# Optimization experiments

Hardware: AMD Instinct MI355X
Metric: run time of the kernel (lower is better)

Reference implementation:

```python
import jax, jax.numpy as jnp
import numpy as np
import math

GROUPS = 32  # min(256 // 4, 32)
EPS = 1e-5

def group_norm(x, w, b):
    B, C, H, W = x.shape
    xg = x.reshape(B, GROUPS, C // GROUPS, H, W)
    mean = jnp.mean(xg, axis=(2, 3, 4), keepdims=True)
    var = jnp.var(xg, axis=(2, 3, 4), keepdims=True)
    xn = ((xg - mean) * jax.lax.rsqrt(var + EPS)).reshape(B, C, H, W)
    return xn * w[None, :, None, None] + b[None, :, None, None]

def nin(x, W, b):
    # 1x1 projection: [B,C,H,W] x [C,D] -> [B,D,H,W]
    return jnp.einsum('bchw,cd->bdhw', x, W) + b[None, :, None, None]

def setup_inputs() -> dict:
    key = jax.random.key(0)
    ks = jax.random.split(key, 5)
    C = 256
    scale = 1.0 / math.sqrt(C)
    return {
        'x': jax.random.normal(ks[0], (4, C, 64, 64), dtype=jnp.float32),
        'gn_w': jnp.ones((C,), jnp.float32),
        'gn_b': jnp.zeros((C,), jnp.float32),
        'Wq': jax.random.normal(ks[1], (C, C), jnp.float32) * scale,
        'bq': jnp.zeros((C,), jnp.float32),
        'Wk': jax.random.normal(ks[2], (C, C), jnp.float32) * scale,
        'bk': jnp.zeros((C,), jnp.float32),
        'Wv': jax.random.normal(ks[3], (C, C), jnp.float32) * scale,
        'bv': jnp.zeros((C,), jnp.float32),
        'Wp': jax.random.normal(ks[4], (C, C), jnp.float32) * scale,
        'bp': jnp.zeros((C,), jnp.float32),
    }

def reference(x, gn_w, gn_b, Wq, bq, Wk, bk, Wv, bv, Wp, bp):
    B, C, H, W = x.shape
    h = group_norm(x, gn_w, gn_b)
    q = nin(h, Wq, bq).reshape(B, C, H * W)
    k = nin(h, Wk, bk).reshape(B, C, H * W)
    v = nin(h, Wv, bv).reshape(B, C, H * W)
    # attention logits: [B, HW, HW]
    w = jnp.einsum('bcn,bcm->bnm', q, k) * (C ** -0.5)
    w = jax.nn.softmax(w, axis=-1)
    h_out = jnp.einsum('bnm,bcm->bcn', w, v).reshape(B, C, H, W)
    h_out = nin(h_out, Wp, bp)
    out = x + h_out
    return out / math.sqrt(2.0)  # skip_rescale=True
```

## Files before the change

### kernel.cpp

```cpp
#include <hip/hip_runtime.h>
#include <math.h>


#define BB 4
#define CCH 256
#define NSP 4096
#define EPSV 1e-5f
#define ATTN_SCALE 0.0625f
#define RSQRT2 0.70710678118654752440f
#define KSPLIT 2
#define TILES_PER_PART 32

typedef __attribute__((ext_vector_type(8))) short bf16x8;
typedef __attribute__((ext_vector_type(4))) float f32x4;

typedef __attribute__((address_space(1))) void gvoid;
typedef __attribute__((address_space(3))) void lvoid;
__device__ __forceinline__ void dma16(const void* g, void* l) {
  __builtin_amdgcn_global_load_lds((gvoid*)g, (lvoid*)l, 16, 0, 0);
}

__device__ __forceinline__ short f2bf(float f) {
  union { float f; unsigned u; } a; a.f = f;
  unsigned r = a.u + 0x7fffu + ((a.u >> 16) & 1u);
  return (short)(r >> 16);
}
__device__ __forceinline__ float bf2f(short s) {
  union { unsigned u; float f; } a;
  a.u = ((unsigned)(unsigned short)s) << 16;
  return a.f;
}
__device__ __forceinline__ unsigned cvt_pk_bf16(float lo, float hi) {
  unsigned r;
  asm("v_cvt_pk_bf16_f32 %0, %1, %2" : "=v"(r) : "v"(lo), "v"(hi));
  return r;
}

__global__ __launch_bounds__(256) void gn_stats(
    const float* __restrict__ x, float* __restrict__ stats) {
  int b = blockIdx.x >> 5;
  int g = blockIdx.x & 31;
  size_t base = ((size_t)b * CCH + (size_t)g * 8) * NSP;
  const float4* xv = (const float4*)(x + base);
  int tid = threadIdx.x;
  float s = 0.f, ss = 0.f;
  for (int i = tid; i < 8192; i += 256) {
    float4 v = xv[i];
    s += (v.x + v.y) + (v.z + v.w);
    ss += (v.x * v.x + v.y * v.y) + (v.z * v.z + v.w * v.w);
  }
#pragma unroll
  for (int off = 32; off > 0; off >>= 1) {
    s += __shfl_down(s, off, 64);
    ss += __shfl_down(ss, off, 64);
  }
  __shared__ float rs[4], rss[4];
  int wv = tid >> 6;
  if ((tid & 63) == 0) { rs[wv] = s; rss[wv] = ss; }
  __syncthreads();
  if (tid == 0) {
    float S = rs[0] + rs[1] + rs[2] + rs[3];
    float SS = rss[0] + rss[1] + rss[2] + rss[3];
    float mean = S * (1.f / 32768.f);
    float var = SS * (1.f / 32768.f) - mean * mean;
    stats[(b * 32 + g) * 2 + 0] = mean;
    stats[(b * 32 + g) * 2 + 1] = rsqrtf(var + EPSV);
  }
}

__global__ __launch_bounds__(256) void prep_w(
    const float* __restrict__ Wq, const float* __restrict__ Wk,
    const float* __restrict__ Wv, const float* __restrict__ Wp,
    short* __restrict__ wts) {
  __shared__ float T[64][65];
  int c0 = blockIdx.x * 64, d0 = blockIdx.y * 64;
  int wz = blockIdx.z;
  const float* W = (wz == 0) ? Wq : (wz == 1) ? Wk : (wz == 2) ? Wv : Wp;
  short* wt = wts + (size_t)wz * CCH * CCH;
  int tid = threadIdx.x;
#pragma unroll
  for (int i = 0; i < 16; ++i) {
    int idx = tid + 256 * i;
    int row = idx >> 6, col = idx & 63;
    T[row][col] = W[(size_t)(c0 + row) * CCH + d0 + col];
  }
  __syncthreads();
#pragma unroll
  for (int i = 0; i < 16; ++i) {
    int idx = tid + 256 * i;
    int dr = idx >> 6, cc = idx & 63;
    wt[(size_t)(d0 + dr) * CCH + c0 + cc] = f2bf(T[cc][dr]);
  }
}

__global__ __launch_bounds__(256) void qkvg_kernel(
    const float* __restrict__ x, const float* __restrict__ stats,
    const float* __restrict__ gw, const float* __restrict__ gb,
    const short* __restrict__ wqt, const short* __restrict__ wkt,
    const short* __restrict__ wvt,
    const float* __restrict__ bq, const float* __restrict__ bk,
    const float* __restrict__ bv,
    short* __restrict__ qo, short* __restrict__ ko, short* __restrict__ vo) {
  __shared__ __align__(16) unsigned char smem[52224];
  float (*Ts)[68] = (float(*)[68])smem;
  float* aco = (float*)(smem + 17408);
  float* bco = aco + 256;
  short* Hs = (short*)(smem + 19456);
  short* Fo = (short*)smem;

  int bx = blockIdx.x;
  int b = bx & 3, n0 = (bx >> 2) * 64;
  int tid = threadIdx.x;
  {
    int g = tid >> 3;
    float mean = stats[(b * 32 + g) * 2 + 0];
    float rstd = stats[(b * 32 + g) * 2 + 1];
    float a = gw[tid] * rstd;
    aco[tid] = a;
    bco[tid] = gb[tid] - mean * a;
  }
  __syncthreads();
  const float* xb = x + (size_t)b * CCH * NSP;
  for (int p = 0; p < 4; ++p) {
    int c0 = p * 64;
#pragma unroll
    for (int i = 0; i < 4; ++i) {
      int crow = (tid >> 4) + i * 16;
      int c = c0 + crow;
      float4 v = *(const float4*)&xb[(size_t)c * NSP + n0 + (tid & 15) * 4];
      float a = aco[c], bb = bco[c];
      v.x = v.x * a + bb; v.y = v.y * a + bb;
      v.z = v.z * a + bb; v.w = v.w * a + bb;
      *(float4*)&Ts[crow][(tid & 15) * 4] = v;
    }
    __syncthreads();
    {
      int n = tid >> 2, seg = tid & 3;
#pragma unroll
      for (int u = 0; u < 2; ++u) {
        int cb = seg * 16 + u * 8;
        bf16x8 r;
#pragma unroll
        for (int j = 0; j < 8; ++j) r[j] = f2bf(Ts[cb + j][n]);
        int chunk = (c0 + cb) >> 3;
        *(bf16x8*)(Hs + n * 256 + ((chunk ^ (n & 7)) * 8)) = r;
      }
    }
    __syncthreads();
  }
  int w = tid >> 6, lane = tid & 63, quad = lane >> 4, l16 = lane & 15;
  bf16x8 a_h[8];
  {
    int row = w * 16 + l16;
#pragma unroll
    for (int kc = 0; kc < 8; ++kc)
      a_h[kc] = *(bf16x8*)(Hs + row * 256 + (((kc * 4 + quad) ^ (row & 7)) * 8));
  }
  __syncthreads();
  for (int op = 0; op < 3; ++op) {
    const short* wt = (op == 0) ? wqt : (op == 1) ? wkt : wvt;
    const float* bias = (op == 0) ? bq : (op == 1) ? bk : bv;
    f32x4 acc[16];
#pragma unroll
    for (int mb = 0; mb < 16; ++mb) acc[mb] = (f32x4){0.f, 0.f, 0.f, 0.f};
#pragma unroll 4
    for (int mb = 0; mb < 16; ++mb) {
      const short* wp = wt + (size_t)(mb * 16 + l16) * CCH + quad * 8;
#pragma unroll
      for (int kc = 0; kc < 8; ++kc) {
        bf16x8 af = *(const bf16x8*)(wp + kc * 32);
        acc[mb] = __builtin_amdgcn_mfma_f32_16x16x32_bf16(af, a_h[kc], acc[mb], 0, 0, 0);
      }
    }
    int n = n0 + w * 16 + l16;
    if (op == 2) {
      short* ob = vo + (size_t)b * CCH * NSP;
      int mm = n & 63, m0_ = n & ~63;
      int mb_ = mm >> 4, qq = (mm >> 2) & 3, rr2 = mm & 3;
      int lc = (mb_ & 1) * 4 + qq;
      int jj = (mb_ >> 1) * 4 + rr2;
      int basen = m0_ + jj;
#pragma unroll
      for (int mb = 0; mb < 16; ++mb)
#pragma unroll
        for (int r = 0; r < 4; ++r) {
          int d = mb * 16 + quad * 4 + r;
          ob[(size_t)d * NSP + basen + ((lc ^ (d & 7)) << 3)] =
              f2bf(acc[mb][r] + bias[d]);
        }
    } else {
      float sc = (op == 0) ? ATTN_SCALE : 1.f;
      int nl = w * 16 + l16;
#pragma unroll
      for (int mb = 0; mb < 16; ++mb)
#pragma unroll
        for (int r = 0; r < 4; ++r) {
          int d = mb * 16 + quad * 4 + r;
          Fo[nl * 264 + d] = f2bf((acc[mb][r] + bias[d]) * sc);
        }
      __syncthreads();
      short* ob = ((op == 0) ? qo : ko) + (size_t)b * NSP * CCH;
#pragma unroll
      for (int it = 0; it < 2; ++it) {
        int idx = tid + 256 * it;
        int row = idx >> 3, seg = idx & 7, r7 = row & 7;
        short* dst = ob + (size_t)(n0 + row) * CCH + seg * 32;
#pragma unroll
        for (int i = 0; i < 4; ++i) {
          int xch = seg * 4 + i;
          int cs = (xch & 24) | ((xch & 7) ^ r7);
          *(bf16x8*)(dst + i * 8) = *(bf16x8*)(Fo + row * 264 + cs * 8);
        }
      }
      __syncthreads();
    }
  }
}

__global__ __launch_bounds__(512, 1) void attn_kernel(
    const short* __restrict__ q, const short* __restrict__ k,
    const short* __restrict__ v, short* __restrict__ po,
    float* __restrict__ pm, float* __restrict__ pl) {
  __shared__ __align__(16) unsigned char smem[65536];
  short* Ks = (short*)smem;
  short* Vs = (short*)(smem + 32768);
  short* Fo = (short*)smem;

  int bx = blockIdx.x;
  int b = bx & 3;
  int n0 = ((bx >> 2) & 31) << 7;
  int kh = bx >> 7;
  const short* qb = q + (size_t)b * NSP * CCH;
  const short* kb = k + (size_t)b * NSP * CCH;
  const char*  vbB = (const char*)(v + (size_t)b * CCH * NSP);
  int tid = threadIdx.x;
  int w = tid >> 6, lane = tid & 63, quad = lane >> 4, l16 = lane & 15;
  int mbase = kh * TILES_PER_PART * 64;

#pragma unroll
  for (int i = 0; i < 4; ++i) {
    int off = tid * 16 + i * 8192;
    int c = off >> 7, inrow = off & 127;
    dma16(vbB + (size_t)c * (NSP * 2) + (size_t)mbase * 2 + inrow,
          (char*)Vs + off);
  }
#pragma unroll
  for (int i = 0; i < 4; ++i) {
    int off = tid * 16 + i * 8192;
    dma16((const char*)(qb + (size_t)n0 * CCH) + off, (char*)Ks + off);
  }
  __syncthreads();
  bf16x8 a_q[8];
  if ((w >> 2) == 0) {
    int row = (w & 3) * 16 + l16;
#pragma unroll
    for (int kc = 0; kc < 8; ++kc)
      a_q[kc] = *(bf16x8*)(Ks + row * 256 + (((kc * 4 + quad) ^ (row & 7)) * 8));
  }
  __syncthreads();
#pragma unroll
  for (int i = 0; i < 4; ++i) {
    int off = tid * 16 + i * 8192;
    dma16((const char*)(qb + (size_t)(n0 + 64) * CCH) + off, (char*)Ks + off);
  }
  __syncthreads();
  if ((w >> 2) == 1) {
    int row = (w & 3) * 16 + l16;
#pragma unroll
    for (int kc = 0; kc < 8; ++kc)
      a_q[kc] = *(bf16x8*)(Ks + row * 256 + (((kc * 4 + quad) ^ (row & 7)) * 8));
  }
  __syncthreads();
#pragma unroll
  for (int i = 0; i < 4; ++i) {
    int off = tid * 16 + i * 8192;
    dma16((const char*)(kb + (size_t)mbase * CCH) + off, (char*)Ks + off);
  }
  __syncthreads();

  f32x4 accO[16];
#pragma unroll
  for (int cb = 0; cb < 16; ++cb) accO[cb] = (f32x4){0.f, 0.f, 0.f, 0.f};
  float m_run = -1e30f, l_run = 0.f;
  int pc0 = quad ^ (l16 & 7);
  int pc1 = (4 + quad) ^ (l16 & 7);

#pragma unroll 1
  for (int t = 0; t < TILES_PER_PART; ++t) {
    f32x4 s[4];
#pragma unroll
    for (int mb = 0; mb < 4; ++mb) s[mb] = (f32x4){0.f, 0.f, 0.f, 0.f};
    __builtin_amdgcn_s_setprio(1);
#pragma unroll
    for (int kc = 0; kc < 8; ++kc) {
#pragma unroll
      for (int mb = 0; mb < 4; ++mb) {
        int row = mb * 16 + l16;
        bf16x8 kf = *(bf16x8*)(Ks + row * 256 + (((kc * 4 + quad) ^ (row & 7)) * 8));
        s[mb] = __builtin_amdgcn_mfma_f32_16x16x32_bf16(kf, a_q[kc], s[mb], 0, 0, 0);
      }
    }
    __builtin_amdgcn_s_setprio(0);
    __syncthreads();
    if (t < TILES_PER_PART - 1) {
      const char* kp = (const char*)(kb + (size_t)(mbase + (t + 1) * 64) * CCH);
#pragma unroll
      for (int i = 0; i < 4; ++i) {
        int off = tid * 16 + i * 8192;
        dma16(kp + off, (char*)Ks + off);
      }
    }
    float mx = -1e30f;
#pragma unroll
    for (int mb = 0; mb < 4; ++mb)
#pragma unroll
      for (int r = 0; r < 4; ++r) mx = fmaxf(mx, s[mb][r]);
    mx = fmaxf(mx, __shfl_xor(mx, 16));
    mx = fmaxf(mx, __shfl_xor(mx, 32));
    if (!__all(mx - m_run <= 8.f)) {
      float mnew = fmaxf(m_run, mx);
      float alpha = __expf(m_run - mnew);
#pragma unroll
      for (int cb = 0; cb < 16; ++cb) accO[cb] *= alpha;
      l_run *= alpha;
      m_run = mnew;
    }
    float ls = 0.f;
#pragma unroll
    for (int mb = 0; mb < 4; ++mb)
#pragma unroll
      for (int r = 0; r < 4; ++r) {
        float p = __expf(s[mb][r] - m_run);
        ls += p;
        s[mb][r] = p;
      }
    ls += __shfl_xor(ls, 16);
    ls += __shfl_xor(ls, 32);
    l_run += ls;
    union { unsigned u[4]; bf16x8 v; } pw0, pw1;
    pw0.u[0] = cvt_pk_bf16(s[0][0], s[0][1]);
    pw0.u[1] = cvt_pk_bf16(s[0][2], s[0][3]);
    pw0.u[2] = cvt_pk_bf16(s[2][0], s[2][1]);
    pw0.u[3] = cvt_pk_bf16(s[2][2], s[2][3]);
    pw1.u[0] = cvt_pk_bf16(s[1][0], s[1][1]);
    pw1.u[1] = cvt_pk_bf16(s[1][2], s[1][3]);
    pw1.u[2] = cvt_pk_bf16(s[3][0], s[3][1]);
    pw1.u[3] = cvt_pk_bf16(s[3][2], s[3][3]);
    __builtin_amdgcn_s_setprio(1);
#pragma unroll
    for (int cb = 0; cb < 16; ++cb) {
      bf16x8 vf = *(bf16x8*)(Vs + (cb * 16 + l16) * 64 + pc0 * 8);
      accO[cb] = __builtin_amdgcn_mfma_f32_16x16x32_bf16(vf, pw0.v, accO[cb], 0, 0, 0);
    }
#pragma unroll
    for (int cb = 0; cb < 16; ++cb) {
      bf16x8 vf = *(bf16x8*)(Vs + (cb * 16 + l16) * 64 + pc1 * 8);
      accO[cb] = __builtin_amdgcn_mfma_f32_16x16x32_bf16(vf, pw1.v, accO[cb], 0, 0, 0);
    }
    __builtin_amdgcn_s_setprio(0);
    __syncthreads();
    if (t < TILES_PER_PART - 1) {
      int m0 = mbase + (t + 1) * 64;
#pragma unroll
      for (int i = 0; i < 4; ++i) {
        int off = tid * 16 + i * 8192;
        int c = off >> 7, inrow = off & 127;
        dma16(vbB + (size_t)c * (NSP * 2) + (size_t)m0 * 2 + inrow,
              (char*)Vs + off);
      }
    }
  }
  size_t sbase = ((size_t)kh * BB + b) * NSP + n0;
  if (quad == 0) {
    pm[sbase + w * 16 + l16] = m_run;
    pl[sbase + w * 16 + l16] = l_run;
  }
  float linv = 1.f / l_run;
  short* ob = po + ((size_t)kh * BB + b) * NSP * CCH;
#pragma unroll
  for (int p = 0; p < 2; ++p) {
    __syncthreads();
    if ((w >> 2) == p) {
      int nloc = (w & 3) * 16 + l16;
#pragma unroll
      for (int cb = 0; cb < 16; ++cb)
#pragma unroll
        for (int r = 0; r < 4; ++r)
          Fo[nloc * 264 + cb * 16 + quad * 4 + r] = f2bf(accO[cb][r] * linv);
    }
    __syncthreads();
    int row = tid >> 3, seg = tid & 7;
    short* dst = ob + (size_t)(n0 + p * 64 + row) * CCH + seg * 32;
#pragma unroll
    for (int i = 0; i < 4; ++i)
      *(bf16x8*)(dst + i * 8) = *(bf16x8*)(Fo + row * 264 + seg * 32 + i * 8);
  }
}

__global__ __launch_bounds__(256) void proj_kernel(
    const short* __restrict__ po, const float* __restrict__ pm,
    const float* __restrict__ pl, const short* __restrict__ wpt,
    const float* __restrict__ bp, const float* __restrict__ x,
    float* __restrict__ out) {
  int n0 = blockIdx.x * 64;
  int dh = blockIdx.y * 128;
  int b = blockIdx.z;
  int tid = threadIdx.x;
  int w = tid >> 6, lane = tid & 63, quad = lane >> 4, l16 = lane & 15;
  int n = n0 + w * 16 + l16;

  float wgt[KSPLIT];
  {
    float m[KSPLIT];
    float M = -1e30f;
#pragma unroll
    for (int s = 0; s < KSPLIT; ++s) {
      m[s] = pm[((size_t)s * BB + b) * NSP + n];
      M = fmaxf(M, m[s]);
    }
    float wsum = 0.f;
#pragma unroll
    for (int s = 0; s < KSPLIT; ++s) {
      wgt[s] = __expf(m[s] - M) * pl[((size_t)s * BB + b) * NSP + n];
      wsum += wgt[s];
    }
    float linv = 1.f / wsum;
#pragma unroll
    for (int s = 0; s < KSPLIT; ++s) wgt[s] *= linv;
  }

  f32x4 acc[8];
#pragma unroll
  for (int mb = 0; mb < 8; ++mb) acc[mb] = (f32x4){0.f, 0.f, 0.f, 0.f};

  const short* pob = po + ((size_t)b * NSP + n) * CCH;
#pragma unroll 2
  for (int kc = 0; kc < 8; ++kc) {
    int coff = kc * 32 + quad * 8;
    float e[8];
#pragma unroll
    for (int i = 0; i < 8; ++i) e[i] = 0.f;
#pragma unroll
    for (int s = 0; s < KSPLIT; ++s) {
      bf16x8 f = *(const bf16x8*)(pob + (size_t)s * BB * NSP * CCH + coff);
#pragma unroll
      for (int i = 0; i < 8; ++i) e[i] += wgt[s] * bf2f(f[i]);
    }
    bf16x8 bm;
#pragma unroll
    for (int i = 0; i < 8; ++i) bm[i] = f2bf(e[i]);
#pragma unroll
    for (int mb = 0; mb < 8; ++mb) {
      bf16x8 af = *(const bf16x8*)(wpt + (size_t)(dh + mb * 16 + l16) * CCH + coff);
      acc[mb] = __builtin_amdgcn_mfma_f32_16x16x32_bf16(af, bm, acc[mb], 0, 0, 0);
    }
  }
#pragma unroll
  for (int mb = 0; mb < 8; ++mb) {
#pragma unroll
    for (int r = 0; r < 4; ++r) {
      int d = dh + mb * 16 + quad * 4 + r;
      size_t off = ((size_t)b * CCH + d) * NSP + n;
      out[off] = (acc[mb][r] + bp[d] + x[off]) * RSQRT2;
    }
  }
}

extern "C" void kernel_launch(void* const* d_in, const int* in_sizes, int n_in,
                              void* d_out, int out_size, void* d_ws, size_t ws_size,
                              hipStream_t stream) {
  const float* x  = (const float*)d_in[0];
  const float* gw = (const float*)d_in[1];
  const float* gb = (const float*)d_in[2];
  const float* Wq = (const float*)d_in[3];
  const float* bq = (const float*)d_in[4];
  const float* Wk = (const float*)d_in[5];
  const float* bk = (const float*)d_in[6];
  const float* Wv = (const float*)d_in[7];
  const float* bv = (const float*)d_in[8];
  const float* Wp = (const float*)d_in[9];
  const float* bp = (const float*)d_in[10];
  float* out = (float*)d_out;

  const size_t SZ = (size_t)BB * CCH * NSP;
  short* qb  = (short*)d_ws;
  short* kb  = qb + SZ;
  short* vb  = kb + SZ;
  short* poT = vb + SZ;
  float* pm  = (float*)(poT + (size_t)KSPLIT * SZ);
  float* pl  = pm + (size_t)KSPLIT * BB * NSP;
  float* stats = pl + (size_t)KSPLIT * BB * NSP;
  short* wts = (short*)(stats + BB * 64);
  short* wqt = wts;
  short* wkt = wts + (size_t)CCH * CCH;
  short* wvt = wts + (size_t)2 * CCH * CCH;
  short* wpt = wts + (size_t)3 * CCH * CCH;

  gn_stats<<<dim3(BB * 32), dim3(256), 0, stream>>>(x, stats);
  prep_w<<<dim3(4, 4, 4), dim3(256), 0, stream>>>(Wq, Wk, Wv, Wp, wts);
  qkvg_kernel<<<dim3(256), dim3(256), 0, stream>>>(
      x, stats, gw, gb, wqt, wkt, wvt, bq, bk, bv, qb, kb, vb);
  attn_kernel<<<dim3(BB * 32 * KSPLIT), dim3(512), 0, stream>>>(
      qb, kb, vb, poT, pm, pl);
  proj_kernel<<<dim3(64, 2, BB), dim3(256), 0, stream>>>(
      poT, pm, pl, wpt, bp, x, out);
}
```

Baseline: 289.0 us.

## Double-buffer K/V in LDS and software-pipeline QK^T one tile ahead

The attention kernel doubles its LDS to hold two K and two V tiles. It computes the QK^T scores for the next tile while the softmax and PV MFMAs for the current tile run, and prefetches K two tiles ahead and V one tile ahead. This cuts the loop to one barrier per iteration and is meant to hide global-load latency and let matrix work overlap the softmax math. In exchange it uses 128KB of LDS and extra registers for the held score tile.

```diff
diff --git a/kernel.cpp b/kernel.cpp
--- a/kernel.cpp
+++ b/kernel.cpp
@@ -221,10 +221,12 @@
     const short* __restrict__ q, const short* __restrict__ k,
     const short* __restrict__ v, short* __restrict__ po,
     float* __restrict__ pm, float* __restrict__ pl) {
-  __shared__ __align__(16) unsigned char smem[65536];
-  short* Ks = (short*)smem;
-  short* Vs = (short*)(smem + 32768);
-  short* Fo = (short*)smem;
+  __shared__ __align__(16) unsigned char smem[131072];
+  short* Ks0 = (short*)smem;
+  short* Ks1 = (short*)(smem + 32768);
+  short* Vs0 = (short*)(smem + 65536);
+  short* Vs1 = (short*)(smem + 98304);
+  short* Fo  = (short*)smem;
 
   int bx = blockIdx.x;
   int b = bx & 3;
@@ -237,46 +239,54 @@
   int w = tid >> 6, lane = tid & 63, quad = lane >> 4, l16 = lane & 15;
   int mbase = kh * TILES_PER_PART * 64;
 
+  bf16x8 a_q[8];
+#pragma unroll
+  for (int p = 0; p < 2; ++p) {
+#pragma unroll
+    for (int i = 0; i < 4; ++i) {
+      int off = tid * 16 + i * 8192;
+      dma16((const char*)(qb + (size_t)(n0 + p * 64) * CCH) + off,
+            (char*)Ks0 + off);
+    }
+    __syncthreads();
+    if ((w >> 2) == p) {
+      int row = (w & 3) * 16 + l16;
+#pragma unroll
+      for (int kc = 0; kc < 8; ++kc)
+        a_q[kc] = *(bf16x8*)(Ks0 + row * 256 + (((kc * 4 + quad) ^ (row & 7)) * 8));
+    }
+    __syncthreads();
+  }
+
 #pragma unroll
   for (int i = 0; i < 4; ++i) {
     int off = tid * 16 + i * 8192;
+    dma16((const char*)(kb + (size_t)mbase * CCH) + off, (char*)Ks0 + off);
     int c = off >> 7, inrow = off & 127;
     dma16(vbB + (size_t)c * (NSP * 2) + (size_t)mbase * 2 + inrow,
-          (char*)Vs + off);
-  }
+          (char*)Vs0 + off);
+  }
+  __syncthreads();
 #pragma unroll
   for (int i = 0; i < 4; ++i) {
     int off = tid * 16 + i * 8192;
-    dma16((const char*)(qb + (size_t)n0 * CCH) + off, (char*)Ks + off);
-  }
-  __syncthreads();
-  bf16x8 a_q[8];
-  if ((w >> 2) == 0) {
-    int row = (w & 3) * 16 + l16;
-#pragma unroll
-    for (int kc = 0; kc < 8; ++kc)
-      a_q[kc] = *(bf16x8*)(Ks + row * 256 + (((kc * 4 + quad) ^ (row & 7)) * 8));
-  }
-  __syncthreads();
-#pragma unroll
-  for (int i = 0; i < 4; ++i) {
-    int off = tid * 16 + i * 8192;
-    dma16((const char*)(qb + (size_t)(n0 + 64) * CCH) + off, (char*)Ks + off);
-  }
-  __syncthreads();
-  if ((w >> 2) == 1) {
-    int row = (w & 3) * 16 + l16;
-#pragma unroll
-    for (int kc = 0; kc < 8; ++kc)
-      a_q[kc] = *(bf16x8*)(Ks + row * 256 + (((kc * 4 + quad) ^ (row & 7)) * 8));
-  }
-  __syncthreads();
-#pragma unroll
-  for (int i = 0; i < 4; ++i) {
-    int off = tid * 16 + i * 8192;
-    dma16((const char*)(kb + (size_t)mbase * CCH) + off, (char*)Ks + off);
-  }
-  __syncthreads();
+    dma16((const char*)(kb + (size_t)(mbase + 64) * CCH) + off,
+          (char*)Ks1 + off);
+  }
+  f32x4 s_prev[4];
+#pragma unroll
+  for (int mb = 0; mb < 4; ++mb) s_prev[mb] = (f32x4){0.f, 0.f, 0.f, 0.f};
+  __builtin_amdgcn_s_setprio(1);
+#pragma unroll
+  for (int kc = 0; kc < 8; ++kc) {
+#pragma unroll
+    for (int mb = 0; mb < 4; ++mb) {
+      int row = mb * 16 + l16;
+      bf16x8 kf = *(bf16x8*)(Ks0 + row * 256 + (((kc * 4 + quad) ^ (row & 7)) * 8));
+      s_prev[mb] = __builtin_amdgcn_mfma_f32_16x16x32_bf16(kf, a_q[kc], s_prev[mb], 0, 0, 0);
+    }
+  }
+  __builtin_amdgcn_s_setprio(0);
 
   f32x4 accO[16];
 #pragma unroll
@@ -287,34 +297,50 @@
 
 #pragma unroll 1
   for (int t = 0; t < TILES_PER_PART; ++t) {
-    f32x4 s[4];
-#pragma unroll
-    for (int mb = 0; mb < 4; ++mb) s[mb] = (f32x4){0.f, 0.f, 0.f, 0.f};
-    __builtin_amdgcn_s_setprio(1);
-#pragma unroll
-    for (int kc = 0; kc < 8; ++kc) {
-#pragma unroll
-      for (int mb = 0; mb < 4; ++mb) {
-        int row = mb * 16 + l16;
-        bf16x8 kf = *(bf16x8*)(Ks + row * 256 + (((kc * 4 + quad) ^ (row & 7)) * 8));
-        s[mb] = __builtin_amdgcn_mfma_f32_16x16x32_bf16(kf, a_q[kc], s[mb], 0, 0, 0);
-      }
-    }
-    __builtin_amdgcn_s_setprio(0);
-    __syncthreads();
-    if (t < TILES_PER_PART - 1) {
-      const char* kp = (const char*)(kb + (size_t)(mbase + (t + 1) * 64) * CCH);
+    __syncthreads();
+    short* Kd = (t & 1) ? Ks1 : Ks0;
+    short* Kr = (t & 1) ? Ks0 : Ks1;
+    short* Vd = (t & 1) ? Vs0 : Vs1;
+    short* Vr = (t & 1) ? Vs1 : Vs0;
+    if (t + 2 < TILES_PER_PART) {
+      const char* kp = (const char*)(kb + (size_t)(mbase + (t + 2) * 64) * CCH);
 #pragma unroll
       for (int i = 0; i < 4; ++i) {
         int off = tid * 16 + i * 8192;
-        dma16(kp + off, (char*)Ks + off);
-      }
+        dma16(kp + off, (char*)Kd + off);
+      }
+    }
+    if (t + 1 < TILES_PER_PART) {
+      int m0 = mbase + (t + 1) * 64;
+#pragma unroll
+      for (int i = 0; i < 4; ++i) {
+        int off = tid * 16 + i * 8192;
+        int c = off >> 7, inrow = off & 127;
+        dma16(vbB + (size_t)c * (NSP * 2) + (size_t)m0 * 2 + inrow,
+              (char*)Vd + off);
+      }
+    }
+    f32x4 sn[4];
+#pragma unroll
+    for (int mb = 0; mb < 4; ++mb) sn[mb] = (f32x4){0.f, 0.f, 0.f, 0.f};
+    if (t + 1 < TILES_PER_PART) {
+      __builtin_amdgcn_s_setprio(1);
+#pragma unroll
+      for (int kc = 0; kc < 8; ++kc) {
+#pragma unroll
+        for (int mb = 0; mb < 4; ++mb) {
+          int row = mb * 16 + l16;
+          bf16x8 kf = *(bf16x8*)(Kr + row * 256 + (((kc * 4 + quad) ^ (row & 7)) * 8));
+          sn[mb] = __builtin_amdgcn_mfma_f32_16x16x32_bf16(kf, a_q[kc], sn[mb], 0, 0, 0);
+        }
+      }
+      __builtin_amdgcn_s_setprio(0);
     }
     float mx = -1e30f;
 #pragma unroll
     for (int mb = 0; mb < 4; ++mb)
 #pragma unroll
-      for (int r = 0; r < 4; ++r) mx = fmaxf(mx, s[mb][r]);
+      for (int r = 0; r < 4; ++r) mx = fmaxf(mx, s_prev[mb][r]);
     mx = fmaxf(mx, __shfl_xor(mx, 16));
     mx = fmaxf(mx, __shfl_xor(mx, 32));
     if (!__all(mx - m_run <= 8.f)) {
@@ -330,45 +356,36 @@
     for (int mb = 0; mb < 4; ++mb)
 #pragma unroll
       for (int r = 0; r < 4; ++r) {
-        float p = __expf(s[mb][r] - m_run);
+        float p = __expf(s_prev[mb][r] - m_run);
         ls += p;
-        s[mb][r] = p;
+        s_prev[mb][r] = p;
       }
     ls += __shfl_xor(ls, 16);
     ls += __shfl_xor(ls, 32);
     l_run += ls;
     union { unsigned u[4]; bf16x8 v; } pw0, pw1;
-    pw0.u[0] = cvt_pk_bf16(s[0][0], s[0][1]);
-    pw0.u[1] = cvt_pk_bf16(s[0][2], s[0][3]);
-    pw0.u[2] = cvt_pk_bf16(s[2][0], s[2][1]);
-    pw0.u[3] = cvt_pk_bf16(s[2][2], s[2][3]);
-    pw1.u[0] = cvt_pk_bf16(s[1][0], s[1][1]);
-    pw1.u[1] = cvt_pk_bf16(s[1][2], s[1][3]);
-    pw1.u[2] = cvt_pk_bf16(s[3][0], s[3][1]);
-    pw1.u[3] = cvt_pk_bf16(s[3][2], s[3][3]);
+    pw0.u[0] = cvt_pk_bf16(s_prev[0][0], s_prev[0][1]);
+    pw0.u[1] = cvt_pk_bf16(s_prev[0][2], s_prev[0][3]);
+    pw0.u[2] = cvt_pk_bf16(s_prev[2][0], s_prev[2][1]);
+    pw0.u[3] = cvt_pk_bf16(s_prev[2][2], s_prev[2][3]);
+    pw1.u[0] = cvt_pk_bf16(s_prev[1][0], s_prev[1][1]);
+    pw1.u[1] = cvt_pk_bf16(s_prev[1][2], s_prev[1][3]);
+    pw1.u[2] = cvt_pk_bf16(s_prev[3][0], s_prev[3][1]);
+    pw1.u[3] = cvt_pk_bf16(s_prev[3][2], s_prev[3][3]);
     __builtin_amdgcn_s_setprio(1);
 #pragma unroll
     for (int cb = 0; cb < 16; ++cb) {
-      bf16x8 vf = *(bf16x8*)(Vs + (cb * 16 + l16) * 64 + pc0 * 8);
+      bf16x8 vf = *(bf16x8*)(Vr + (cb * 16 + l16) * 64 + pc0 * 8);
       accO[cb] = __builtin_amdgcn_mfma_f32_16x16x32_bf16(vf, pw0.v, accO[cb], 0, 0, 0);
     }
 #pragma unroll
     for (int cb = 0; cb < 16; ++cb) {
-      bf16x8 vf = *(bf16x8*)(Vs + (cb * 16 + l16) * 64 + pc1 * 8);
+      bf16x8 vf = *(bf16x8*)(Vr + (cb * 16 + l16) * 64 + pc1 * 8);
       accO[cb] = __builtin_amdgcn_mfma_f32_16x16x32_bf16(vf, pw1.v, accO[cb], 0, 0, 0);
     }
     __builtin_amdgcn_s_setprio(0);
-    __syncthreads();
-    if (t < TILES_PER_PART - 1) {
-      int m0 = mbase + (t + 1) * 64;
-#pragma unroll
-      for (int i = 0; i < 4; ++i) {
-        int off = tid * 16 + i * 8192;
-        int c = off >> 7, inrow = off & 127;
-        dma16(vbB + (size_t)c * (NSP * 2) + (size_t)m0 * 2 + inrow,
-              (char*)Vs + off);
-      }
-    }
+#pragma unroll
+    for (int mb = 0; mb < 4; ++mb) s_prev[mb] = sn[mb];
   }
   size_t sbase = ((size_t)kh * BB + b) * NSP + n0;
   if (quad == 0) {
```

Result: faster. 282.9 us (-2.1%).

## Rebalance attention to 64-query blocks with two blocks per CU, widen QKV blocks

Applied to the files above, without the earlier changes.

The attention kernel moves from 512-thread blocks covering 128 queries (one block per CU) to 256-thread blocks covering 64 queries, with twice as many blocks and launch bounds allowing two per CU. This removes the two-phase Q staging and the split epilogue. The QKV projection kernel now uses 512 threads per block, with the output channels split into two halves across wave groups, which halves the accumulators per wave. The aim is better occupancy and latency hiding, at the cost of reloading each K/V tile for twice as many query blocks and a tighter register budget.

```diff
diff --git a/kernel.cpp b/kernel.cpp
--- a/kernel.cpp
+++ b/kernel.cpp
@@ -93,7 +93,7 @@
   }
 }
 
-__global__ __launch_bounds__(256) void qkvg_kernel(
+__global__ __launch_bounds__(512) void qkvg_kernel(
     const float* __restrict__ x, const float* __restrict__ stats,
     const float* __restrict__ gw, const float* __restrict__ gb,
     const short* __restrict__ wqt, const short* __restrict__ wkt,
@@ -111,7 +111,7 @@
   int bx = blockIdx.x;
   int b = bx & 3, n0 = (bx >> 2) * 64;
   int tid = threadIdx.x;
-  {
+  if (tid < 256) {
     int g = tid >> 3;
     float mean = stats[(b * 32 + g) * 2 + 0];
     float rstd = stats[(b * 32 + g) * 2 + 1];
@@ -124,8 +124,8 @@
   for (int p = 0; p < 4; ++p) {
     int c0 = p * 64;
 #pragma unroll
-    for (int i = 0; i < 4; ++i) {
-      int crow = (tid >> 4) + i * 16;
+    for (int i = 0; i < 2; ++i) {
+      int crow = (tid >> 4) + i * 32;
       int c = c0 + crow;
       float4 v = *(const float4*)&xb[(size_t)c * NSP + n0 + (tid & 15) * 4];
       float a = aco[c], bb = bco[c];
@@ -135,23 +135,21 @@
     }
     __syncthreads();
     {
-      int n = tid >> 2, seg = tid & 3;
-#pragma unroll
-      for (int u = 0; u < 2; ++u) {
-        int cb = seg * 16 + u * 8;
-        bf16x8 r;
-#pragma unroll
-        for (int j = 0; j < 8; ++j) r[j] = f2bf(Ts[cb + j][n]);
-        int chunk = (c0 + cb) >> 3;
-        *(bf16x8*)(Hs + n * 256 + ((chunk ^ (n & 7)) * 8)) = r;
-      }
+      int n = tid >> 3, seg = tid & 7;
+      int cb = seg * 8;
+      bf16x8 r;
+#pragma unroll
+      for (int j = 0; j < 8; ++j) r[j] = f2bf(Ts[cb + j][n]);
+      int chunk = (c0 + cb) >> 3;
+      *(bf16x8*)(Hs + n * 256 + ((chunk ^ (n & 7)) * 8)) = r;
     }
     __syncthreads();
   }
   int w = tid >> 6, lane = tid & 63, quad = lane >> 4, l16 = lane & 15;
+  int wr = w & 3, h = w >> 2;
   bf16x8 a_h[8];
   {
-    int row = w * 16 + l16;
+    int row = wr * 16 + l16;
 #pragma unroll
     for (int kc = 0; kc < 8; ++kc)
       a_h[kc] = *(bf16x8*)(Hs + row * 256 + (((kc * 4 + quad) ^ (row & 7)) * 8));
@@ -160,19 +158,19 @@
   for (int op = 0; op < 3; ++op) {
     const short* wt = (op == 0) ? wqt : (op == 1) ? wkt : wvt;
     const float* bias = (op == 0) ? bq : (op == 1) ? bk : bv;
-    f32x4 acc[16];
-#pragma unroll
-    for (int mb = 0; mb < 16; ++mb) acc[mb] = (f32x4){0.f, 0.f, 0.f, 0.f};
+    f32x4 acc[8];
+#pragma unroll
+    for (int mb = 0; mb < 8; ++mb) acc[mb] = (f32x4){0.f, 0.f, 0.f, 0.f};
 #pragma unroll 4
-    for (int mb = 0; mb < 16; ++mb) {
-      const short* wp = wt + (size_t)(mb * 16 + l16) * CCH + quad * 8;
+    for (int mb = 0; mb < 8; ++mb) {
+      const short* wp = wt + (size_t)((h * 8 + mb) * 16 + l16) * CCH + quad * 8;
 #pragma unroll
       for (int kc = 0; kc < 8; ++kc) {
         bf16x8 af = *(const bf16x8*)(wp + kc * 32);
         acc[mb] = __builtin_amdgcn_mfma_f32_16x16x32_bf16(af, a_h[kc], acc[mb], 0, 0, 0);
       }
     }
-    int n = n0 + w * 16 + l16;
+    int n = n0 + wr * 16 + l16;
     if (op == 2) {
       short* ob = vo + (size_t)b * CCH * NSP;
       int mm = n & 63, m0_ = n & ~63;
@@ -181,29 +179,27 @@
       int jj = (mb_ >> 1) * 4 + rr2;
       int basen = m0_ + jj;
 #pragma unroll
-      for (int mb = 0; mb < 16; ++mb)
+      for (int mb = 0; mb < 8; ++mb)
 #pragma unroll
         for (int r = 0; r < 4; ++r) {
-          int d = mb * 16 + quad * 4 + r;
+          int d = (h * 8 + mb) * 16 + quad * 4 + r;
           ob[(size_t)d * NSP + basen + ((lc ^ (d & 7)) << 3)] =
               f2bf(acc[mb][r] + bias[d]);
         }
     } else {
       float sc = (op == 0) ? ATTN_SCALE : 1.f;
-      int nl = w * 16 + l16;
-#pragma unroll
-      for (int mb = 0; mb < 16; ++mb)
+      int nl = wr * 16 + l16;
+#pragma unroll
+      for (int mb = 0; mb < 8; ++mb)
 #pragma unroll
         for (int r = 0; r < 4; ++r) {
-          int d = mb * 16 + quad * 4 + r;
+          int d = (h * 8 + mb) * 16 + quad * 4 + r;
           Fo[nl * 264 + d] = f2bf((acc[mb][r] + bias[d]) * sc);
         }
       __syncthreads();
       short* ob = ((op == 0) ? qo : ko) + (size_t)b * NSP * CCH;
-#pragma unroll
-      for (int it = 0; it < 2; ++it) {
-        int idx = tid + 256 * it;
-        int row = idx >> 3, seg = idx & 7, r7 = row & 7;
+      {
+        int row = tid >> 3, seg = tid & 7, r7 = row & 7;
         short* dst = ob + (size_t)(n0 + row) * CCH + seg * 32;
 #pragma unroll
         for (int i = 0; i < 4; ++i) {
@@ -217,7 +213,7 @@
   }
 }
 
-__global__ __launch_bounds__(512, 1) void attn_kernel(
+__global__ __launch_bounds__(256, 2) void attn_kernel(
     const short* __restrict__ q, const short* __restrict__ k,
     const short* __restrict__ v, short* __restrict__ po,
     float* __restrict__ pm, float* __restrict__ pl) {
@@ -227,9 +223,10 @@
   short* Fo = (short*)smem;
 
   int bx = blockIdx.x;
-  int b = bx & 3;
-  int n0 = ((bx >> 2) & 31) << 7;
-  int kh = bx >> 7;
+  int grp = bx & 7;
+  int b = grp & 3;
+  int kh = grp >> 2;
+  int n0 = (bx >> 3) << 6;
   const short* qb = q + (size_t)b * NSP * CCH;
   const short* kb = k + (size_t)b * NSP * CCH;
   const char*  vbB = (const char*)(v + (size_t)b * CCH * NSP);
@@ -238,43 +235,27 @@
   int mbase = kh * TILES_PER_PART * 64;
 
 #pragma unroll
-  for (int i = 0; i < 4; ++i) {
-    int off = tid * 16 + i * 8192;
+  for (int i = 0; i < 8; ++i) {
+    int off = tid * 16 + i * 4096;
+    dma16((const char*)(qb + (size_t)n0 * CCH) + off, (char*)Ks + off);
+  }
+  __syncthreads();
+  bf16x8 a_q[8];
+  {
+    int row = w * 16 + l16;
+#pragma unroll
+    for (int kc = 0; kc < 8; ++kc)
+      a_q[kc] = *(bf16x8*)(Ks + row * 256 + (((kc * 4 + quad) ^ (row & 7)) * 8));
+  }
+  __syncthreads();
+
+#pragma unroll
+  for (int i = 0; i < 8; ++i) {
+    int off = tid * 16 + i * 4096;
+    dma16((const char*)(kb + (size_t)mbase * CCH) + off, (char*)Ks + off);
     int c = off >> 7, inrow = off & 127;
     dma16(vbB + (size_t)c * (NSP * 2) + (size_t)mbase * 2 + inrow,
           (char*)Vs + off);
-  }
-#pragma unroll
-  for (int i = 0; i < 4; ++i) {
-    int off = tid * 16 + i * 8192;
-    dma16((const char*)(qb + (size_t)n0 * CCH) + off, (char*)Ks + off);
-  }
-  __syncthreads();
-  bf16x8 a_q[8];
-  if ((w >> 2) == 0) {
-    int row = (w & 3) * 16 + l16;
-#pragma unroll
-    for (int kc = 0; kc < 8; ++kc)
-      a_q[kc] = *(bf16x8*)(Ks + row * 256 + (((kc * 4 + quad) ^ (row & 7)) * 8));
-  }
-  __syncthreads();
-#pragma unroll
-  for (int i = 0; i < 4; ++i) {
-    int off = tid * 16 + i * 8192;
-    dma16((const char*)(qb + (size_t)(n0 + 64) * CCH) + off, (char*)Ks + off);
-  }
-  __syncthreads();
-  if ((w >> 2) == 1) {
-    int row = (w & 3) * 16 + l16;
-#pragma unroll
-    for (int kc = 0; kc < 8; ++kc)
-      a_q[kc] = *(bf16x8*)(Ks + row * 256 + (((kc * 4 + quad) ^ (row & 7)) * 8));
-  }
-  __syncthreads();
-#pragma unroll
-  for (int i = 0; i < 4; ++i) {
-    int off = tid * 16 + i * 8192;
-    dma16((const char*)(kb + (size_t)mbase * CCH) + off, (char*)Ks + off);
   }
   __syncthreads();
 
@@ -302,11 +283,11 @@
     }
     __builtin_amdgcn_s_setprio(0);
     __syncthreads();
-    if (t < TILES_PER_PART - 1) {
+    if (t + 1 < TILES_PER_PART) {
       const char* kp = (const char*)(kb + (size_t)(mbase + (t + 1) * 64) * CCH);
 #pragma unroll
-      for (int i = 0; i < 4; ++i) {
-        int off = tid * 16 + i * 8192;
+      for (int i = 0; i < 8; ++i) {
+        int off = tid * 16 + i * 4096;
         dma16(kp + off, (char*)Ks + off);
       }
     }
@@ -359,11 +340,11 @@
     }
     __builtin_amdgcn_s_setprio(0);
     __syncthreads();
-    if (t < TILES_PER_PART - 1) {
+    if (t + 1 < TILES_PER_PART) {
       int m0 = mbase + (t + 1) * 64;
 #pragma unroll
-      for (int i = 0; i < 4; ++i) {
-        int off = tid * 16 + i * 8192;
+      for (int i = 0; i < 8; ++i) {
+        int off = tid * 16 + i * 4096;
         int c = off >> 7, inrow = off & 127;
         dma16(vbB + (size_t)c * (NSP * 2) + (size_t)m0 * 2 + inrow,
               (char*)Vs + off);
@@ -377,23 +358,21 @@
   }
   float linv = 1.f / l_run;
   short* ob = po + ((size_t)kh * BB + b) * NSP * CCH;
-#pragma unroll
-  for (int p = 0; p < 2; ++p) {
-    __syncthreads();
-    if ((w >> 2) == p) {
-      int nloc = (w & 3) * 16 + l16;
-#pragma unroll
-      for (int cb = 0; cb < 16; ++cb)
-#pragma unroll
-        for (int r = 0; r < 4; ++r)
-          Fo[nloc * 264 + cb * 16 + quad * 4 + r] = f2bf(accO[cb][r] * linv);
-    }
-    __syncthreads();
-    int row = tid >> 3, seg = tid & 7;
-    short* dst = ob + (size_t)(n0 + p * 64 + row) * CCH + seg * 32;
-#pragma unroll
-    for (int i = 0; i < 4; ++i)
-      *(bf16x8*)(dst + i * 8) = *(bf16x8*)(Fo + row * 264 + seg * 32 + i * 8);
+  {
+    int nloc = w * 16 + l16;
+#pragma unroll
+    for (int cb = 0; cb < 16; ++cb)
+#pragma unroll
+      for (int r = 0; r < 4; ++r)
+        Fo[nloc * 264 + cb * 16 + quad * 4 + r] = f2bf(accO[cb][r] * linv);
+  }
+  __syncthreads();
+  {
+    int row = tid >> 2, seg = tid & 3;
+    short* dst = ob + (size_t)(n0 + row) * CCH + seg * 64;
+#pragma unroll
+    for (int i = 0; i < 8; ++i)
+      *(bf16x8*)(dst + i * 8) = *(bf16x8*)(Fo + row * 264 + seg * 64 + i * 8);
   }
 }
 
@@ -498,9 +477,9 @@
 
   gn_stats<<<dim3(BB * 32), dim3(256), 0, stream>>>(x, stats);
   prep_w<<<dim3(4, 4, 4), dim3(256), 0, stream>>>(Wq, Wk, Wv, Wp, wts);
-  qkvg_kernel<<<dim3(256), dim3(256), 0, stream>>>(
+  qkvg_kernel<<<dim3(256), dim3(512), 0, stream>>>(
       x, stats, gw, gb, wqt, wkt, wvt, bq, bk, bv, qb, kb, vb);
-  attn_kernel<<<dim3(BB * 32 * KSPLIT), dim3(512), 0, stream>>>(
+  attn_kernel<<<dim3(BB * 64 * KSPLIT), dim3(256), 0, stream>>>(
       qb, kb, vb, poT, pm, pl);
   proj_kernel<<<dim3(64, 2, BB), dim3(256), 0, stream>>>(
       poT, pm, pl, wpt, bp, x, out);
```

Result: faster. 283.2 us (-2.0%).
